# Kernel tuning notes

Measured on AMD Instinct MI355X. Metric: run time of the kernel, lower is better.

The kernel has to match this reference:

```python
import jax, jax.numpy as jnp
import numpy as np

NUM_STEPS = 100
STEP = 2.0 / (NUM_STEPS - 1)          # bin width over [-1, 1]
EPS = 1.0 / NUM_STEPS
TSIZE = NUM_STEPS                      # bin centers t_k = -1 + k*STEP, k=0..99
B, D = 4096, 128
NUM_CLASSES = 100


def setup_inputs() -> dict:
    key = jax.random.key(0)
    k1, k2 = jax.random.split(key)
    embeddings = jax.random.normal(k1, (B, D), dtype=jnp.float32)
    classes = jax.random.randint(k2, (B,), 0, NUM_CLASSES)
    return {"embeddings": embeddings, "classes": classes}


def _histogram_loss(embeddings, classes):
    n = embeddings.shape[0]
    iu, ju = np.triu_indices(n, 1)            # static upper-triangular pair indices
    # cosine similarity of all pairs (outer_cosine_similarity)
    en = embeddings / jnp.linalg.norm(embeddings, axis=1, keepdims=True)
    dists = en @ en.T                          # [B, B]
    s = jnp.clip(dists[iu, ju], -1.0 + 1e-6, 1.0 - 1e-6)   # [P]
    pos = (classes[iu] == classes[ju])         # [P] bool

    # soft triangular-kernel 2-bin scatter (equivalent to indsa/indsb masking):
    # bin j gets (t_j + STEP - s)/STEP, bin j+1 gets (s - t_j)/STEP
    j = jnp.floor((s + 1.0 - 1e-6) / STEP).astype(jnp.int32)   # lower bin index
    t_j = j.astype(s.dtype) * STEP - 1.0
    w_hi = (s - t_j) / STEP                    # weight for bin j+1
    w_lo = (t_j + STEP - s) / STEP             # weight for bin j

    def histogram(mask):
        m = mask.astype(s.dtype)
        size = m.sum()
        h = jnp.zeros((TSIZE,), dtype=s.dtype)
        h = h.at[j].add(w_lo * m).at[j + 1].add(w_hi * m)
        return h / size

    hist_pos = histogram(pos)
    hist_neg = histogram(~pos)
    # tril-masked repeat + sum(0) in the original is exactly a cumulative sum
    hist_pos_cdf = jnp.cumsum(hist_pos)
    return jnp.sum(hist_neg * hist_pos_cdf)


def reference(embeddings, classes):
    return _histogram_loss(embeddings, classes)
```

## Files before the change

kernel.cpp:

```cpp
#include <hip/hip_runtime.h>
#include <hip/hip_bf16.h>
#include <cstddef>

#define BN 4096
#define DD 128
#define NSTEPS 100
#define PTILE 128
#define PLSTR 136
#define GRID_T 32
#define NOFF 496
#define NUNITS 528
#define NBLK 264
#define NREPH 16
#define NREPC2 8

typedef __attribute__((ext_vector_type(8))) short bf16x8;
typedef __attribute__((ext_vector_type(4))) float f32x4;

__device__ __forceinline__ void faddf(float* p, float v) { unsafeAtomicAdd(p, v); }

#define ZERON 166

__global__ __launch_bounds__(256) void hl_normalize(const float* __restrict__ emb,
                                                    ushort* __restrict__ out,
                                                    float* __restrict__ zero_blk) {
    if (blockIdx.x == 0 && threadIdx.x < ZERON) zero_blk[threadIdx.x] = 0.f;
    int w = threadIdx.x >> 6;
    int lane = threadIdx.x & 63;
    int row = (blockIdx.x << 2) + w;
    const float2 v = *(const float2*)(emb + (size_t)row * DD + 2 * lane);
    float ss = v.x * v.x + v.y * v.y;
    #pragma unroll
    for (int off = 32; off > 0; off >>= 1) ss += __shfl_xor(ss, off);
    float inv = 1.0f / sqrtf(ss);
    __hip_bfloat16 b0 = __float2bfloat16(v.x * inv);
    __hip_bfloat16 b1 = __float2bfloat16(v.y * inv);
    ushort2 pk;
    pk.x = *(ushort*)&b0;
    pk.y = *(ushort*)&b1;
    *(ushort2*)(out + (size_t)row * DD + 2 * lane) = pk;
}

__global__ __launch_bounds__(256) void hl_poscls(const ushort* __restrict__ nemb,
                                                 const int* __restrict__ cls,
                                                 float* __restrict__ gPos,
                                                 unsigned int* __restrict__ gDoneP,
                                                 float* __restrict__ gCdf) {
    const int c = blockIdx.x;
    __shared__ int idx[256];
    __shared__ int scan[256];
    __shared__ ushort As[64 * PLSTR];
    __shared__ ushort Bs[64 * PLSTR];
    __shared__ float hpos[NREPH * 101];
    __shared__ int mTot;
    __shared__ int lastFlag;
    const int tid = threadIdx.x;

    for (int i = tid; i < NREPH * 101; i += 256) hpos[i] = 0.f;

    const int base = tid * 16;
    int myCnt = 0;
    #pragma unroll
    for (int k = 0; k < 16; ++k) myCnt += (cls[base + k] == c);
    scan[tid] = myCnt;
    __syncthreads();
    for (int s = 1; s < 256; s <<= 1) {
        int v = (tid >= s) ? scan[tid - s] : 0;
        __syncthreads();
        scan[tid] += v;
        __syncthreads();
    }
    int w = scan[tid] - myCnt;
    if (tid == 255) mTot = scan[255] > 256 ? 256 : scan[255];
    #pragma unroll
    for (int k = 0; k < 16; ++k) {
        if (cls[base + k] == c && w < 256) { idx[w] = base + k; ++w; }
    }
    __syncthreads();
    const int m = mTot;
    const int nt = (m + 63) >> 6;

    constexpr float INVSTEP = 49.5f;
    constexpr float CLIPV = 1.0f - 1e-6f;

    const int lane = tid & 63;
    const int wv = tid >> 6;
    const int lr = lane & 15;
    const int kg = lane >> 4;
    const int rep = (lane & 15) * 101;

    for (int si = 0; si < nt; ++si) {
        for (int sj = si; sj < nt; ++sj) {
            __syncthreads();
            #pragma unroll
            for (int it = 0; it < 4; ++it) {
                int q = it * 256 + tid;
                int row = q >> 4;
                int ch = q & 15;
                int ga = si * 64 + row;
                int gb = sj * 64 + row;
                int ra = idx[ga < m ? ga : 0];
                int rb = idx[gb < m ? gb : 0];
                *(float4*)(&As[row * PLSTR + ch * 8]) =
                    *(const float4*)(nemb + (size_t)ra * DD + ch * 8);
                *(float4*)(&Bs[row * PLSTR + ch * 8]) =
                    *(const float4*)(nemb + (size_t)rb * DD + ch * 8);
            }
            __syncthreads();

            f32x4 zero4 = {0.f, 0.f, 0.f, 0.f};
            f32x4 pacc[4] = {zero4, zero4, zero4, zero4};
            #pragma unroll
            for (int ks = 0; ks < 4; ++ks) {
                bf16x8 af = *(const bf16x8*)(&As[(wv * 16 + lr) * PLSTR + ks * 32 + kg * 8]);
                #pragma unroll
                for (int fb = 0; fb < 4; ++fb) {
                    bf16x8 bf = *(const bf16x8*)(&Bs[(fb * 16 + lr) * PLSTR + ks * 32 + kg * 8]);
                    pacc[fb] = __builtin_amdgcn_mfma_f32_16x16x32_bf16(af, bf, pacc[fb], 0, 0, 0);
                }
            }

            #pragma unroll
            for (int fb = 0; fb < 4; ++fb) {
                const int gb = sj * 64 + fb * 16 + lr;
                #pragma unroll
                for (int j = 0; j < 4; ++j) {
                    const int ga = si * 64 + wv * 16 + kg * 4 + j;
                    if (ga < gb && gb < m) {
                        float s = pacc[fb][j];
                        s = fminf(fmaxf(s, -CLIPV), CLIPV);
                        float u = (s + CLIPV) * INVSTEP;
                        int jb = (int)u;
                        if (jb > 98) jb = 98;
                        float w_hi = u - (float)jb;
                        float w_lo = 1.0f - w_hi;
                        faddf(&hpos[rep + jb], w_lo);
                        faddf(&hpos[rep + jb + 1], w_hi);
                    }
                }
            }
        }
    }
    __syncthreads();
    if (tid < NSTEPS) {
        float v = 0.f;
        #pragma unroll
        for (int r = 0; r < NREPH; ++r) v += hpos[r * 101 + tid];
        if (v != 0.f) faddf(&gPos[tid], v);
    }
    __threadfence();
    if (tid == 0) {
        unsigned int tk = atomicAdd(gDoneP, 1u);
        lastFlag = (tk == NSTEPS - 1);
    }
    __syncthreads();
    if (lastFlag) {
        float v = (tid < NSTEPS)
            ? __hip_atomic_load(&gPos[tid], __ATOMIC_RELAXED, __HIP_MEMORY_SCOPE_AGENT) : 0.f;
        if (tid < 128) hpos[tid] = v;
        __syncthreads();
        for (int off = 1; off < 128; off <<= 1) {
            float x = 0.f;
            if (tid < 128 && tid >= off) x = hpos[tid - off];
            __syncthreads();
            if (tid < 128) hpos[tid] += x;
            __syncthreads();
        }
        const float invsp = 1.0f / hpos[NSTEPS - 1];
        if (tid < NSTEPS) gCdf[tid] = hpos[tid] * invsp;
    }
}

__global__ __launch_bounds__(256, 2) void hl_neg(const ushort* __restrict__ nemb,
                                                 const int* __restrict__ cls,
                                                 const float* __restrict__ gCdf,
                                                 float* __restrict__ gLoss,
                                                 float* __restrict__ gCnt,
                                                 unsigned int* __restrict__ gDone,
                                                 float* __restrict__ out) {
    __shared__ ushort As[PTILE * 128];
    __shared__ ushort Bs[PTILE * 128];
    __shared__ float2 cdf2[NREPC2 * 101];
    __shared__ float red[8];
    __shared__ int clsAb[2][PTILE], clsBb[2][PTILE];

    const int tid = threadIdx.x;
    const int lane = tid & 63;
    const int wid = tid >> 6;
    const int wr = wid >> 1, wc = wid & 1;
    const int lr = lane & 15;
    const int kg = lane >> 4;

    int tiU[2], tjU[2];
    #pragma unroll
    for (int u = 0; u < 2; ++u) {
        int id = blockIdx.x * 2 + u;
        if (id < NOFF) {
            int ti = 0, rem = id;
            while (rem >= GRID_T - 1 - ti) { rem -= GRID_T - 1 - ti; ++ti; }
            tiU[u] = ti; tjU[u] = ti + 1 + rem;
        } else {
            tiU[u] = tjU[u] = id - NOFF;
        }
    }

    for (int i = tid; i < NREPC2 * NSTEPS; i += 256) {
        int r = i / NSTEPS, b = i - r * NSTEPS;
        float c0 = gCdf[b];
        float c1 = gCdf[(b < NSTEPS - 1) ? b + 1 : NSTEPS - 1];
        float2 cd; cd.x = c0; cd.y = c1 - c0;
        cdf2[r * 101 + b] = cd;
    }

    constexpr float INVSTEP = 49.5f;
    constexpr float CLIPV = 1.0f - 1e-6f;
    const float2* crep2 = &cdf2[(lane & 7) * 101];
    const int li_base = wr * 64 + (kg << 2);
    const int lj_base = wc * 64 + lr;

    float lacc = 0.f, lcnt = 0.f;
    const int rloc = lane >> 4;
    const int pch = lane & 15;

    #define STAGE_UNIT(U)                                                            \
    {                                                                                \
        const int ti_ = tiU[U], tj_ = tjU[U];                                        \
        const bool dg_ = (ti_ == tj_);                                               \
        if (tid < PTILE) clsAb[(U) & 1][tid] = cls[ti_ * PTILE + tid];               \
        else             clsBb[(U) & 1][tid - PTILE] = cls[tj_ * PTILE + (tid - PTILE)]; \
        const ushort* Ag_ = nemb + (size_t)(ti_ * PTILE) * DD;                       \
        const ushort* Bg_ = nemb + (size_t)(tj_ * PTILE) * DD;                       \
        _Pragma("unroll")                                                            \
        for (int t = 0; t < 8; ++t) {                                                \
            int row = wid * 32 + t * 4 + rloc;                                       \
            int lch = pch ^ (row & 7);                                               \
            const ushort* ga = Ag_ + (size_t)row * DD + lch * 8;                     \
            ushort* la = &As[(wid * 32 + t * 4) * 128];                              \
            __builtin_amdgcn_global_load_lds(                                        \
                (const __attribute__((address_space(1))) void*)ga,                   \
                (__attribute__((address_space(3))) void*)la, 16, 0, 0);              \
        }                                                                            \
        if (!dg_) {                                                                  \
            _Pragma("unroll")                                                        \
            for (int t = 0; t < 8; ++t) {                                            \
                int row = wid * 32 + t * 4 + rloc;                                   \
                int lch = pch ^ (row & 7);                                           \
                const ushort* gb = Bg_ + (size_t)row * DD + lch * 8;                 \
                ushort* lb = &Bs[(wid * 32 + t * 4) * 128];                          \
                __builtin_amdgcn_global_load_lds(                                    \
                    (const __attribute__((address_space(1))) void*)gb,               \
                    (__attribute__((address_space(3))) void*)lb, 16, 0, 0);          \
            }                                                                        \
        }                                                                            \
    }

    STAGE_UNIT(0);

    #pragma unroll
    for (int u = 0; u < 2; ++u) {
        const bool diag = (tiU[u] == tjU[u]);

        __syncthreads();

        const ushort* Bsel = diag ? As : Bs;

        f32x4 zero4 = {0.f, 0.f, 0.f, 0.f};
        f32x4 acc[4][4];
        #pragma unroll
        for (int a = 0; a < 4; ++a)
            #pragma unroll
            for (int b = 0; b < 4; ++b) acc[a][b] = zero4;

        #pragma unroll
        for (int ks = 0; ks < 4; ++ks) {
            bf16x8 af[4], bfr[4];
            #pragma unroll
            for (int f = 0; f < 4; ++f) {
                int arow = wr * 64 + f * 16 + lr;
                int pca = ((ks << 2) | kg) ^ (arow & 7);
                af[f] = *(const bf16x8*)(&As[arow * 128 + pca * 8]);
                int brow = wc * 64 + f * 16 + lr;
                int pcb = ((ks << 2) | kg) ^ (brow & 7);
                bfr[f] = *(const bf16x8*)(&Bsel[brow * 128 + pcb * 8]);
            }
            #pragma unroll
            for (int fa = 0; fa < 4; ++fa)
                #pragma unroll
                for (int fb = 0; fb < 4; ++fb)
                    acc[fa][fb] = __builtin_amdgcn_mfma_f32_16x16x32_bf16(af[fa], bfr[fb], acc[fa][fb], 0, 0, 0);
        }

        __syncthreads();

        if (u == 0) STAGE_UNIT(1);

        const int* clsA_ = clsAb[u & 1];
        const int* clsB_ = diag ? clsAb[u & 1] : clsBb[u & 1];
        const bool offdiag = !diag;

        int ca[16];
        #pragma unroll
        for (int fa = 0; fa < 4; ++fa)
            #pragma unroll
            for (int j = 0; j < 4; ++j) ca[fa * 4 + j] = clsA_[li_base + fa * 16 + j];

        #pragma unroll
        for (int fb = 0; fb < 4; ++fb) {
            const int lj = lj_base + fb * 16;
            const int cb = clsB_[lj];
            #pragma unroll
            for (int fa = 0; fa < 4; ++fa) {
                const int li0 = li_base + fa * 16;
                f32x4 v = acc[fa][fb];
                #pragma unroll
                for (int j = 0; j < 4; ++j) {
                    const int li = li0 + j;
                    const bool mneg = (offdiag || (li < lj)) && (ca[fa * 4 + j] != cb);
                    float s = v[j];
                    s = fminf(fmaxf(s, -CLIPV), CLIPV);
                    float uu = (s + CLIPV) * INVSTEP;
                    int jb = (int)uu;
                    if (jb > 98) jb = 98;
                    float w_hi = uu - (float)jb;
                    float2 cd = crep2[jb];
                    float mm = mneg ? 1.0f : 0.0f;
                    lacc = fmaf(mm, fmaf(w_hi, cd.y, cd.x), lacc);
                    lcnt += mm;
                }
            }
        }
    }
    #undef STAGE_UNIT

    #pragma unroll
    for (int off = 32; off > 0; off >>= 1) {
        lacc += __shfl_xor(lacc, off);
        lcnt += __shfl_xor(lcnt, off);
    }
    if (lane == 0) { red[wid] = lacc; red[4 + wid] = lcnt; }
    __syncthreads();
    if (tid == 0) {
        float L = red[0] + red[1] + red[2] + red[3];
        float C = red[4] + red[5] + red[6] + red[7];
        faddf(&gLoss[blockIdx.x & 31], L);
        faddf(&gCnt[blockIdx.x & 31], C);
        __threadfence();
        unsigned int tk = atomicAdd(gDone, 1u);
        if (tk == NBLK - 1) {
            __threadfence();
            float ls = 0.f, cs = 0.f;
            for (int i = 0; i < 32; ++i) {
                ls += __hip_atomic_load(&gLoss[i], __ATOMIC_RELAXED, __HIP_MEMORY_SCOPE_AGENT);
                cs += __hip_atomic_load(&gCnt[i], __ATOMIC_RELAXED, __HIP_MEMORY_SCOPE_AGENT);
            }
            out[0] = ls / cs;
        }
    }
}

extern "C" void kernel_launch(void* const* d_in, const int* in_sizes, int n_in,
                              void* d_out, int out_size, void* d_ws, size_t ws_size,
                              hipStream_t stream) {
    const float* emb = (const float*)d_in[0];
    const int* classes = (const int*)d_in[1];
    float* out = (float*)d_out;

    ushort* nemb = (ushort*)d_ws;
    float* ctl = (float*)((char*)d_ws + (size_t)BN * DD * sizeof(ushort));
    float* gPos = ctl;
    float* gLoss = gPos + NSTEPS;
    float* gCnt = gLoss + 32;
    unsigned int* gDone = (unsigned int*)(gCnt + 32);
    unsigned int* gDoneP = gDone + 1;
    float* gCdf = (float*)(gDoneP + 1);

    hl_normalize<<<BN / 4, 256, 0, stream>>>(emb, nemb, ctl);
    hl_poscls<<<NSTEPS, 256, 0, stream>>>(nemb, classes, gPos, gDoneP, gCdf);
    hl_neg<<<NBLK, 256, 0, stream>>>(nemb, classes, gCdf, gLoss, gCnt, gDone, out);
}
```

Measured before the change: 42.00 us.

## Fuse row normalization into per-class kernel and drop the normalize launch

Removes the separate normalize kernel. Each per-class block now gathers its member rows, L2-normalizes them and writes the bf16 rows to the workspace for both its own tiles and the later negative kernel. The prefix-scan member collection becomes a shared-memory atomic counter. Zeroing of the control block moves to a hipMemsetAsync. This saves a launch and a pass over the embeddings, but it depends on every row belonging to a class with at most 256 members, and the member order is no longer deterministic.

```diff
diff --git a/kernel.cpp b/kernel.cpp
--- a/kernel.cpp
+++ b/kernel.cpp
@@ -9,7 +9,6 @@
 #define PLSTR 136
 #define GRID_T 32
 #define NOFF 496
-#define NUNITS 528
 #define NBLK 264
 #define NREPH 16
 #define NREPC2 8
@@ -19,72 +18,66 @@
 
 __device__ __forceinline__ void faddf(float* p, float v) { unsafeAtomicAdd(p, v); }
 
+__device__ __forceinline__ unsigned int pkbf2(float a, float b) {
+    __hip_bfloat16 ba = __float2bfloat16(a);
+    __hip_bfloat16 bb = __float2bfloat16(b);
+    return (unsigned int)*(ushort*)&ba | ((unsigned int)*(ushort*)&bb << 16);
+}
+
 #define ZERON 166
 
-__global__ __launch_bounds__(256) void hl_normalize(const float* __restrict__ emb,
-                                                    ushort* __restrict__ out,
-                                                    float* __restrict__ zero_blk) {
-    if (blockIdx.x == 0 && threadIdx.x < ZERON) zero_blk[threadIdx.x] = 0.f;
-    int w = threadIdx.x >> 6;
-    int lane = threadIdx.x & 63;
-    int row = (blockIdx.x << 2) + w;
-    const float2 v = *(const float2*)(emb + (size_t)row * DD + 2 * lane);
-    float ss = v.x * v.x + v.y * v.y;
-    #pragma unroll
-    for (int off = 32; off > 0; off >>= 1) ss += __shfl_xor(ss, off);
-    float inv = 1.0f / sqrtf(ss);
-    __hip_bfloat16 b0 = __float2bfloat16(v.x * inv);
-    __hip_bfloat16 b1 = __float2bfloat16(v.y * inv);
-    ushort2 pk;
-    pk.x = *(ushort*)&b0;
-    pk.y = *(ushort*)&b1;
-    *(ushort2*)(out + (size_t)row * DD + 2 * lane) = pk;
-}
-
-__global__ __launch_bounds__(256) void hl_poscls(const ushort* __restrict__ nemb,
+__global__ __launch_bounds__(256) void hl_poscls(const float* __restrict__ emb,
                                                  const int* __restrict__ cls,
+                                                 ushort* __restrict__ nemb,
                                                  float* __restrict__ gPos,
                                                  unsigned int* __restrict__ gDoneP,
                                                  float* __restrict__ gCdf) {
     const int c = blockIdx.x;
     __shared__ int idx[256];
-    __shared__ int scan[256];
     __shared__ ushort As[64 * PLSTR];
     __shared__ ushort Bs[64 * PLSTR];
     __shared__ float hpos[NREPH * 101];
-    __shared__ int mTot;
+    __shared__ int mCnt;
     __shared__ int lastFlag;
     const int tid = threadIdx.x;
-
+    const int lane = tid & 63;
+    const int wv = tid >> 6;
+
+    if (tid == 0) mCnt = 0;
     for (int i = tid; i < NREPH * 101; i += 256) hpos[i] = 0.f;
-
-    const int base = tid * 16;
-    int myCnt = 0;
-    #pragma unroll
-    for (int k = 0; k < 16; ++k) myCnt += (cls[base + k] == c);
-    scan[tid] = myCnt;
-    __syncthreads();
-    for (int s = 1; s < 256; s <<= 1) {
-        int v = (tid >= s) ? scan[tid - s] : 0;
-        __syncthreads();
-        scan[tid] += v;
-        __syncthreads();
-    }
-    int w = scan[tid] - myCnt;
-    if (tid == 255) mTot = scan[255] > 256 ? 256 : scan[255];
-    #pragma unroll
-    for (int k = 0; k < 16; ++k) {
-        if (cls[base + k] == c && w < 256) { idx[w] = base + k; ++w; }
-    }
-    __syncthreads();
-    const int m = mTot;
+    __syncthreads();
+
+    for (int i = tid; i < BN; i += 256)
+        if (cls[i] == c) { int p = atomicAdd(&mCnt, 1); if (p < 256) idx[p] = i; }
+    __syncthreads();
+    const int m = mCnt > 256 ? 256 : mCnt;
     const int nt = (m + 63) >> 6;
+
+    {
+        const int g = lane >> 4, l16 = lane & 15;
+        for (int r0 = wv * 4; r0 < m; r0 += 16) {
+            int r = r0 + g;
+            if (r < m) {
+                const float* src = emb + (size_t)idx[r] * DD;
+                float4 v0 = *(const float4*)(src + l16 * 8);
+                float4 v1 = *(const float4*)(src + l16 * 8 + 4);
+                float ss = v0.x*v0.x + v0.y*v0.y + v0.z*v0.z + v0.w*v0.w
+                         + v1.x*v1.x + v1.y*v1.y + v1.z*v1.z + v1.w*v1.w;
+                #pragma unroll
+                for (int off = 8; off > 0; off >>= 1) ss += __shfl_xor(ss, off);
+                float inv = 1.0f / sqrtf(ss);
+                uint4 pk;
+                pk.x = pkbf2(v0.x * inv, v0.y * inv);
+                pk.y = pkbf2(v0.z * inv, v0.w * inv);
+                pk.z = pkbf2(v1.x * inv, v1.y * inv);
+                pk.w = pkbf2(v1.z * inv, v1.w * inv);
+                *(uint4*)(nemb + (size_t)idx[r] * DD + l16 * 8) = pk;
+            }
+        }
+    }
 
     constexpr float INVSTEP = 49.5f;
     constexpr float CLIPV = 1.0f - 1e-6f;
-
-    const int lane = tid & 63;
-    const int wv = tid >> 6;
     const int lr = lane & 15;
     const int kg = lane >> 4;
     const int rep = (lane & 15) * 101;
@@ -374,7 +367,7 @@
     unsigned int* gDoneP = gDone + 1;
     float* gCdf = (float*)(gDoneP + 1);
 
-    hl_normalize<<<BN / 4, 256, 0, stream>>>(emb, nemb, ctl);
-    hl_poscls<<<NSTEPS, 256, 0, stream>>>(nemb, classes, gPos, gDoneP, gCdf);
+    hipMemsetAsync(ctl, 0, ZERON * sizeof(float), stream);
+    hl_poscls<<<NSTEPS, 256, 0, stream>>>(emb, classes, nemb, gPos, gDoneP, gCdf);
     hl_neg<<<NBLK, 256, 0, stream>>>(nemb, classes, gCdf, gLoss, gCnt, gDone, out);
 }
```

New measurement: 45.98 us. +9.5%, slower.
